# Kernel tuning notes

Hardware: AMD Instinct MI355X
Metric: run time of the kernel (lower is better)

## Reference

```python
import jax, jax.numpy as jnp
import numpy as np

G = 64          # voxel grid side
N_IN = 150000   # input points
N_OUT = 150000  # output points
K = 3           # cubic kernel size
CIN = 32
FOUT = 64


def _make_cloud(rng, n):
    flat = rng.permutation(G ** 3)[:n]
    x = flat % G
    y = (flat // G) % G
    z = flat // (G * G)
    pos = np.stack([x, y, z], axis=-1).astype(np.float32) + 0.5  # voxel centers
    return flat, pos


def setup_inputs() -> dict:
    rng = np.random.default_rng(0)
    flat_in, inp_pos = _make_cloud(rng, N_IN)
    _, out_pos = _make_cloud(np.random.default_rng(1), N_OUT)

    # Fixed-radius (Linf, r = K*voxel*0.51 = 1.53) search on the grid ==
    # 3x3x3 voxel neighborhood lookup. Build dense voxel -> point-index map.
    grid = np.full(G ** 3, -1, dtype=np.int64)
    grid[flat_in] = np.arange(N_IN)
    offs = np.stack(np.meshgrid(*([np.arange(-1, 2)] * 3), indexing='ij'), -1).reshape(-1, 3)  # [27,3]
    out_vox = (out_pos - 0.5).astype(np.int64)              # [M,3]
    nb = out_vox[:, None, :] + offs[None, :, :]             # [M,27,3]
    inb = ((nb >= 0) & (nb < G)).all(-1)                    # [M,27]
    flat = nb[..., 0] + G * nb[..., 1] + G * G * nb[..., 2]
    flat = np.where(inb, flat, 0)
    found = grid[flat]
    mask = inb & (found >= 0)
    nbr_idx = np.where(mask, found, 0).astype(np.int32)

    key = jax.random.key(0)
    k1, k2, k3, k4, k5 = jax.random.split(key, 5)
    return {
        'inp_features': jax.random.normal(k1, (N_IN, CIN), jnp.float32),
        'inp_positions': jnp.asarray(inp_pos),
        'out_positions': jnp.asarray(out_pos),
        'voxel_size': jnp.asarray(1.0, jnp.float32),
        'inp_importance': jax.random.uniform(k2, (N_IN,), jnp.float32),
        'kernel': jax.random.uniform(k3, (K, K, K, CIN, FOUT), jnp.float32, -0.05, 0.05),
        'bias': jnp.zeros((FOUT,), jnp.float32) + 0.01 * jax.random.normal(k4, (FOUT,)),
        'neighbor_index': jnp.asarray(nbr_idx),
        'neighbor_mask': jnp.asarray(mask),
    }


def _sparse_conv(inp_features, inp_positions, out_positions, voxel_size,
                 inp_importance, kernel, bias, neighbor_index, neighbor_mask):
    # offset = 0 (odd kernel). extent = kernel_size * voxel_size.
    extent = K * voxel_size
    nbr_pos = inp_positions[neighbor_index]                  # [M,Kn,3]
    rel = nbr_pos - out_positions[:, None, :]                # [M,Kn,3]
    # identity coordinate mapping: normalize to [-1,1] over the extent
    n = 2.0 * rel / extent
    # align_corners=False mapping to filter coords, + offset (=0)
    fcoord = (n * 0.5 + 0.5) * K - 0.5                        # [M,Kn,3] (x,y,z)
    idx = jnp.clip(jnp.round(fcoord).astype(jnp.int32), 0, K - 1)
    # kernel is indexed [z,y,x,cin,cout]; positions are [x,y,z]
    flat_cell = idx[..., 2] * (K * K) + idx[..., 1] * K + idx[..., 0]   # [M,Kn]
    onehot = jax.nn.one_hot(flat_cell, K ** 3, dtype=inp_features.dtype)  # [M,Kn,27]
    w = (inp_importance[neighbor_index] * neighbor_mask.astype(inp_features.dtype))  # [M,Kn]
    feat = inp_features[neighbor_index] * w[..., None]       # [M,Kn,Cin]
    # accumulate neighbor features into their kernel cell, then contract with kernel
    cellfeat = jnp.einsum('mko,mkc->moc', onehot, feat)      # [M,27,Cin]
    wflat = kernel.reshape(K ** 3, CIN, FOUT)
    out = jnp.einsum('moc,ocf->mf', cellfeat, wflat)         # [M,F]
    return out + bias


def reference(inp_features, inp_positions, out_positions, voxel_size,
              inp_importance, kernel, bias, neighbor_index, neighbor_mask):
    return _sparse_conv(inp_features, inp_positions, out_positions, voxel_size,
                        inp_importance, kernel, bias, neighbor_index, neighbor_mask)
```

## Files before the change

kernel.cpp:

```cpp
#include <hip/hip_runtime.h>
#include <hip/hip_bf16.h>

#define CELLS 27
#define CIN   32
#define FOUT  64
#define M_OUT 150000
#define N_INP 150000
#define GDIM  64
#define NVOX  (GDIM * GDIM * GDIM)

#define GFEAT_SHORTS (NVOX * CIN)
#define GFEAT_BYTES  (GFEAT_SHORTS * 2)
#define OUTMAP_BYTES (NVOX * 4)
#define WT2_SHORTS   (CELLS * 4 * 64 * 8)
#define WT2_BYTES    (WT2_SHORTS * 2)
#define DENSE_WS     ((size_t)GFEAT_BYTES + OUTMAP_BYTES + WT2_BYTES)

#define CHB   16032
#define LDSSZ (4 * CHB)

#define ZROW  N_INP
#define PPG   64
#define GROUPS ((M_OUT + PPG - 1) / PPG)
#define FB_ROWS  (N_INP + 1)
#define FB_BYTES (FB_ROWS * CIN * 2)

typedef __attribute__((ext_vector_type(4))) float f32x4;
typedef __attribute__((ext_vector_type(8))) short bf16x8;

__device__ __forceinline__ short f2bf(float x) {
    union { __hip_bfloat16 h; short s; } u;
    u.h = __float2bfloat16(x);
    return u.s;
}


__global__ __launch_bounds__(256) void build_kernel(const float* __restrict__ feat,
                                                    const float* __restrict__ ipos,
                                                    const float* __restrict__ opos,
                                                    const float* __restrict__ imp,
                                                    const float* __restrict__ W,
                                                    unsigned short* __restrict__ gfeat,
                                                    int* __restrict__ outmap,
                                                    unsigned short* __restrict__ Wt2) {
    int t = blockIdx.x * 256 + threadIdx.x;
    if (t < N_INP * 4) {
        int p = t >> 2, c = t & 3;
        int x = (int)ipos[p * 3 + 0];
        int y = (int)ipos[p * 3 + 1];
        int z = (int)ipos[p * 3 + 2];
        int flat = x + (y << 6) + (z << 12);
        float wv = imp[p];
        const float* fp = feat + (size_t)p * CIN + c * 8;
        f32x4 f0 = *(const f32x4*)fp;
        f32x4 f1 = *(const f32x4*)(fp + 4);
        bf16x8 o;
        o[0] = f2bf(f0.x * wv); o[1] = f2bf(f0.y * wv);
        o[2] = f2bf(f0.z * wv); o[3] = f2bf(f0.w * wv);
        o[4] = f2bf(f1.x * wv); o[5] = f2bf(f1.y * wv);
        o[6] = f2bf(f1.z * wv); o[7] = f2bf(f1.w * wv);
        *(bf16x8*)(gfeat + (size_t)flat * CIN + c * 8) = o;
    } else if (t < N_INP * 4 + M_OUT) {
        int m = t - N_INP * 4;
        int x = (int)opos[m * 3 + 0];
        int y = (int)opos[m * 3 + 1];
        int z = (int)opos[m * 3 + 2];
        outmap[x + (y << 6) + (z << 12)] = m;
    } else {
        int v = t - (N_INP * 4 + M_OUT);
        if (v < CELLS * 4 * 64) {
            int l    = v & 63;
            int ct   = v >> 6;
            int tt   = ct & 3;
            int cell = ct >> 2;
            int fout = tt * 16 + (l & 15);
            int cin0 = (l >> 4) * 8;
            bf16x8 o;
#pragma unroll
            for (int j = 0; j < 8; ++j)
                o[j] = f2bf(W[cell * 2048 + (cin0 + j) * 64 + fout]);
            *(bf16x8*)(Wt2 + (size_t)v * 8) = o;
        }
    }
}

__global__ __launch_bounds__(512, 4) void conv_dense8_kernel(
        const unsigned short* __restrict__ gfeat,
        const int*   __restrict__ outmap,
        const unsigned short* __restrict__ Wt2,
        const float* __restrict__ bias,
        float* __restrict__ out) {
    __shared__ __align__(16) unsigned char sh[LDSSZ];

    const int tid = threadIdx.x;
    const int bid = blockIdx.x;
    const int bx0 = (bid & 7) * 8;
    const int by0 = ((bid >> 3) & 7) * 8;
    const int bz0 = (bid >> 6) * 8;

    bf16x8 hv[8];
#pragma unroll
    for (int it = 0; it < 8; ++it) {
        int c = it * 512 + tid;
        bf16x8 val = {0, 0, 0, 0, 0, 0, 0, 0};
        if (c < 4000) {
            int v = c >> 2, ch = c & 3;
            int q10  = (v * 6554) >> 16;
            int hx   = v - q10 * 10;
            int q100 = (q10 * 6554) >> 16;
            int hy   = q10 - q100 * 10;
            int hz   = q100;
            int gx = bx0 - 1 + hx, gy = by0 - 1 + hy, gz = bz0 - 1 + hz;
            if (((unsigned)gx < 64u) & ((unsigned)gy < 64u) & ((unsigned)gz < 64u)) {
                int flat = gx + (gy << 6) + (gz << 12);
                val = *(const bf16x8*)(gfeat + (size_t)flat * CIN + ch * 8);
            }
        }
        hv[it] = val;
    }
#pragma unroll
    for (int it = 0; it < 8; ++it) {
        int c = it * 512 + tid;
        if (c < 4000) {
            int v = c >> 2, ch = c & 3;
            *(bf16x8*)&sh[ch * CHB + v * 16] = hv[it];
        }
    }
    __syncthreads();

    const int w    = tid >> 6;
    const int lane = tid & 63;
    const int r = lane & 15;
    const int g = lane >> 4;

    const unsigned char* Ab = sh + g * CHB + ((r & 7) + (r >> 3) * 10 + w * 100) * 16;
    const unsigned short* Bp = Wt2 + lane * 8;

    f32x4 acc[4][4];
#pragma unroll
    for (int mt = 0; mt < 4; ++mt)
#pragma unroll
        for (int nt = 0; nt < 4; ++nt) acc[mt][nt] = (f32x4){0.f, 0.f, 0.f, 0.f};

    bf16x8 bb[2][4];
#pragma unroll
    for (int nt = 0; nt < 4; ++nt)
        bb[0][nt] = *(const bf16x8*)(Bp + nt * 512);

#pragma unroll
    for (int cell = 0; cell < CELLS; ++cell) {
        const int cur = cell & 1, nxt = cur ^ 1;
        const int cx = cell % 3, cy = (cell / 3) % 3, cz = cell / 9;
        if (cell + 1 < CELLS) {
#pragma unroll
            for (int nt = 0; nt < 4; ++nt)
                bb[nxt][nt] = *(const bf16x8*)(Bp + (cell + 1) * 2048 + nt * 512);
        }
#pragma unroll
        for (int mt = 0; mt < 4; ++mt) {
            bf16x8 a = *(const bf16x8*)(Ab + (cx + (cy + 2 * mt) * 10 + cz * 100) * 16);
#pragma unroll
            for (int nt = 0; nt < 4; ++nt)
                acc[mt][nt] = __builtin_amdgcn_mfma_f32_16x16x32_bf16(a, bb[cur][nt],
                                                                      acc[mt][nt], 0, 0, 0);
        }
    }

    float bv0 = bias[r], bv1 = bias[16 + r], bv2 = bias[32 + r], bv3 = bias[48 + r];
#pragma unroll
    for (int mt = 0; mt < 4; ++mt) {
#pragma unroll
        for (int j = 0; j < 4; ++j) {
            int p  = mt * 16 + g * 4 + j;
            int px = p & 7, py = p >> 3;
            int om = outmap[(bx0 + px) + ((by0 + py) << 6) + ((bz0 + w) << 12)];
            if (om >= 0) {
                float* op = out + (size_t)om * FOUT + r;
                op[0]  = acc[mt][0][j] + bv0;
                op[16] = acc[mt][1][j] + bv1;
                op[32] = acc[mt][2][j] + bv2;
                op[48] = acc[mt][3][j] + bv3;
            }
        }
    }
}


#define CELL_OF(k) (((k) % 3) * 9 + (((k) / 3) % 3) * 3 + ((k) / 9))

__global__ __launch_bounds__(256) void prep_fb_kernel(const float* __restrict__ W,
                                                      const float* __restrict__ feat,
                                                      const float* __restrict__ imp,
                                                      unsigned short* __restrict__ Wt2,
                                                      unsigned short* __restrict__ fb) {
    int t = blockIdx.x * 256 + threadIdx.x;
    if (t < FB_ROWS * 4) {
        int i = t >> 2, c = t & 3;
        bf16x8 o = {0, 0, 0, 0, 0, 0, 0, 0};
        if (i < N_INP) {
            float w = imp[i];
            const float* fp = feat + (size_t)i * CIN + c * 8;
            f32x4 f0 = *(const f32x4*)fp;
            f32x4 f1 = *(const f32x4*)(fp + 4);
            o[0] = f2bf(f0.x * w); o[1] = f2bf(f0.y * w);
            o[2] = f2bf(f0.z * w); o[3] = f2bf(f0.w * w);
            o[4] = f2bf(f1.x * w); o[5] = f2bf(f1.y * w);
            o[6] = f2bf(f1.z * w); o[7] = f2bf(f1.w * w);
        }
        *(bf16x8*)(fb + (size_t)i * CIN + c * 8) = o;
    } else {
        int v = t - FB_ROWS * 4;
        if (v < CELLS * 4 * 64) {
            int l    = v & 63;
            int ct   = v >> 6;
            int tt   = ct & 3;
            int cell = ct >> 2;
            int fout = tt * 16 + (l & 15);
            int cin0 = (l >> 4) * 8;
            bf16x8 o;
#pragma unroll
            for (int j = 0; j < 8; ++j)
                o[j] = f2bf(W[cell * 2048 + (cin0 + j) * 64 + fout]);
            *(bf16x8*)(Wt2 + (size_t)v * 8) = o;
        }
    }
}

__global__ __launch_bounds__(128, 4) void conv64_kernel(
        const float* __restrict__ opos,
        const float* __restrict__ ipos,
        const int*   __restrict__ nbr,
        const unsigned short* __restrict__ Wt2,
        const unsigned short* __restrict__ fb,
        const float* __restrict__ bias,
        float* __restrict__ out) {
    __shared__ int s_idx[PPG][28];
    __shared__ int s_vox[PPG];
    __shared__ __align__(16) unsigned char s_A[2][4 * 1056];

    const int tid   = threadIdx.x;
    const int lane  = tid & 63;
    const int fhalf = tid >> 6;
    const int m0    = blockIdx.x * PPG;

    const int vx0 = (int)ipos[0];
    const int vy0 = (int)ipos[1];
    const int vz0 = (int)ipos[2];

    if (fhalf == 0) {
        int m = m0 + lane;
        int vp = -1;
        if (m < M_OUT) {
            vp = ((int)opos[m * 3 + 0] + 1) |
                 (((int)opos[m * 3 + 1] + 1) << 8) |
                 (((int)opos[m * 3 + 2] + 1) << 16);
        }
        s_vox[lane] = vp;
    }
    __syncthreads();

#pragma unroll
    for (int it = 0; it < 14; ++it) {
        int e = it * 128 + tid;
        if (e < CELLS * PPG) {
            int p = e / CELLS;
            int k = e - p * CELLS;
            int m = m0 + p;
            int id = (m < M_OUT) ? nbr[m * CELLS + k] : 0;
            int ox = k / 9, oy = (k / 3) % 3, oz = k % 3;
            int tgt = (vx0 - ox + 2) | ((vy0 - oy + 2) << 8) | ((vz0 - oz + 2) << 16);
            bool valid = (id != 0) | (s_vox[p] == tgt);
            s_idx[p][k] = valid ? id : ZROW;
        }
    }
    __syncthreads();

    const int st_c  = lane & 3;
    const int st_r0 = fhalf * 32 + (lane >> 2);
    const int st_r1 = st_r0 + 16;
    const unsigned short* fb_c = fb + st_c * 8;

    const int g = lane >> 4;
    const int r = lane & 15;
    const int wbase = fhalf * 2;

    {
        int i0 = s_idx[st_r0][0];
        int i1 = s_idx[st_r1][0];
        bf16x8 v0 = *(const bf16x8*)(fb_c + (size_t)i0 * CIN);
        bf16x8 v1 = *(const bf16x8*)(fb_c + (size_t)i1 * CIN);
        *(bf16x8*)&s_A[0][st_c * 1056 + st_r0 * 16] = v0;
        *(bf16x8*)&s_A[0][st_c * 1056 + st_r1 * 16] = v1;
    }
    bf16x8 cb0 = *(const bf16x8*)(Wt2 + (CELL_OF(0) * 4 + wbase + 0) * 512 + lane * 8);
    bf16x8 cb1 = *(const bf16x8*)(Wt2 + (CELL_OF(0) * 4 + wbase + 1) * 512 + lane * 8);
    __syncthreads();

    f32x4 acc[8];
#pragma unroll
    for (int i = 0; i < 8; ++i) acc[i] = (f32x4){0.f, 0.f, 0.f, 0.f};

#pragma unroll
    for (int k = 0; k < CELLS; ++k) {
        const int b = k & 1;
        bf16x8 v0, v1, nb0, nb1;
        const bool more = (k + 1 < CELLS);
        if (more) {
            int i0 = s_idx[st_r0][k + 1];
            int i1 = s_idx[st_r1][k + 1];
            v0 = *(const bf16x8*)(fb_c + (size_t)i0 * CIN);
            v1 = *(const bf16x8*)(fb_c + (size_t)i1 * CIN);
            const int c2 = CELL_OF(k + 1);
            nb0 = *(const bf16x8*)(Wt2 + (c2 * 4 + wbase + 0) * 512 + lane * 8);
            nb1 = *(const bf16x8*)(Wt2 + (c2 * 4 + wbase + 1) * 512 + lane * 8);
        }
        const unsigned char* Ab = &s_A[b][0];
        bf16x8 a0 = *(const bf16x8*)(Ab + g * 1056 +   0 + r * 16);
        bf16x8 a1 = *(const bf16x8*)(Ab + g * 1056 + 256 + r * 16);
        bf16x8 a2 = *(const bf16x8*)(Ab + g * 1056 + 512 + r * 16);
        bf16x8 a3 = *(const bf16x8*)(Ab + g * 1056 + 768 + r * 16);
        acc[0] = __builtin_amdgcn_mfma_f32_16x16x32_bf16(a0, cb0, acc[0], 0, 0, 0);
        acc[1] = __builtin_amdgcn_mfma_f32_16x16x32_bf16(a0, cb1, acc[1], 0, 0, 0);
        acc[2] = __builtin_amdgcn_mfma_f32_16x16x32_bf16(a1, cb0, acc[2], 0, 0, 0);
        acc[3] = __builtin_amdgcn_mfma_f32_16x16x32_bf16(a1, cb1, acc[3], 0, 0, 0);
        acc[4] = __builtin_amdgcn_mfma_f32_16x16x32_bf16(a2, cb0, acc[4], 0, 0, 0);
        acc[5] = __builtin_amdgcn_mfma_f32_16x16x32_bf16(a2, cb1, acc[5], 0, 0, 0);
        acc[6] = __builtin_amdgcn_mfma_f32_16x16x32_bf16(a3, cb0, acc[6], 0, 0, 0);
        acc[7] = __builtin_amdgcn_mfma_f32_16x16x32_bf16(a3, cb1, acc[7], 0, 0, 0);
        if (more) {
            *(bf16x8*)&s_A[b ^ 1][st_c * 1056 + st_r0 * 16] = v0;
            *(bf16x8*)&s_A[b ^ 1][st_c * 1056 + st_r1 * 16] = v1;
            cb0 = nb0;
            cb1 = nb1;
        }
        __syncthreads();
    }

    float bb0 = bias[fhalf * 32 + r];
    float bb1 = bias[fhalf * 32 + 16 + r];
#pragma unroll
    for (int h = 0; h < 4; ++h) {
        int base = m0 + h * 16 + 4 * g;
#pragma unroll
        for (int j = 0; j < 4; ++j) {
            int m = base + j;
            if (m < M_OUT) {
                float* op = out + (size_t)m * FOUT + fhalf * 32 + r;
                op[0]  = acc[h * 2 + 0][j] + bb0;
                op[16] = acc[h * 2 + 1][j] + bb1;
            }
        }
    }
}


extern "C" void kernel_launch(void* const* d_in, const int* in_sizes, int n_in,
                              void* d_out, int out_size, void* d_ws, size_t ws_size,
                              hipStream_t stream) {
    const float* feat = (const float*)d_in[0];
    const float* ipos = (const float*)d_in[1];
    const float* opos = (const float*)d_in[2];
    const float* imp  = (const float*)d_in[4];
    const float* W    = (const float*)d_in[5];
    const float* bias = (const float*)d_in[6];
    const int*   nbr  = (const int*)d_in[7];
    float* out = (float*)d_out;

    if (ws_size >= DENSE_WS) {
        unsigned short* gfeat = (unsigned short*)d_ws;
        int* outmap = (int*)((char*)d_ws + GFEAT_BYTES);
        unsigned short* Wt2 = (unsigned short*)((char*)d_ws + GFEAT_BYTES + OUTMAP_BYTES);

        hipMemsetAsync(gfeat, 0x00, GFEAT_BYTES, stream);
        hipMemsetAsync(outmap, 0xFF, OUTMAP_BYTES, stream);
        int build_threads = N_INP * 4 + M_OUT + CELLS * 4 * 64;
        hipLaunchKernelGGL(build_kernel, dim3((build_threads + 255) / 256), dim3(256),
                           0, stream, feat, ipos, opos, imp, W, gfeat, outmap, Wt2);
        hipLaunchKernelGGL(conv_dense8_kernel, dim3(512), dim3(512), 0, stream,
                           gfeat, outmap, Wt2, bias, out);
    } else {
        unsigned short* Wt2 = (unsigned short*)d_ws;
        unsigned short* fb  = (unsigned short*)((char*)d_ws + WT2_BYTES);
        int prep_threads = FB_ROWS * 4 + CELLS * 4 * 64;
        hipLaunchKernelGGL(prep_fb_kernel, dim3((prep_threads + 255) / 256), dim3(256),
                           0, stream, W, feat, imp, Wt2, fb);
        hipLaunchKernelGGL(conv64_kernel, dim3(GROUPS), dim3(128), 0, stream,
                           opos, ipos, nbr, Wt2, fb, bias, out);
    }
}
```

Before: 156.9 us.

## Stage per-cell weight tiles through double-buffered LDS instead of per-wave global loads

```diff
diff --git a/kernel.cpp b/kernel.cpp
--- a/kernel.cpp
+++ b/kernel.cpp
@@ -16,8 +16,10 @@
 #define WT2_BYTES    (WT2_SHORTS * 2)
 #define DENSE_WS     ((size_t)GFEAT_BYTES + OUTMAP_BYTES + WT2_BYTES)
 
-#define CHB   16032
-#define LDSSZ (4 * CHB)
+#define CHB      16032
+#define BBUF0    (4 * CHB)
+#define BBUFSZ   4128
+#define LDSSZ    (BBUF0 + 2 * BBUFSZ)
 
 #define ZROW  N_INP
 #define PPG   64
@@ -100,32 +102,38 @@
 
     bf16x8 hv[8];
 #pragma unroll
-    for (int it = 0; it < 8; ++it) {
-        int c = it * 512 + tid;
-        bf16x8 val = {0, 0, 0, 0, 0, 0, 0, 0};
-        if (c < 4000) {
-            int v = c >> 2, ch = c & 3;
-            int q10  = (v * 6554) >> 16;
-            int hx   = v - q10 * 10;
-            int q100 = (q10 * 6554) >> 16;
-            int hy   = q10 - q100 * 10;
-            int hz   = q100;
-            int gx = bx0 - 1 + hx, gy = by0 - 1 + hy, gz = bz0 - 1 + hz;
-            if (((unsigned)gx < 64u) & ((unsigned)gy < 64u) & ((unsigned)gz < 64u)) {
-                int flat = gx + (gy << 6) + (gz << 12);
-                val = *(const bf16x8*)(gfeat + (size_t)flat * CIN + ch * 8);
+    for (int ch = 0; ch < 4; ++ch) {
+#pragma unroll
+        for (int h = 0; h < 2; ++h) {
+            int v = h * 512 + tid;
+            bf16x8 val = {0, 0, 0, 0, 0, 0, 0, 0};
+            if (v < 1000) {
+                int q10  = (v * 6554) >> 16;
+                int hx   = v - q10 * 10;
+                int q100 = (q10 * 6554) >> 16;
+                int hy   = q10 - q100 * 10;
+                int hz   = q100;
+                int gx = bx0 - 1 + hx, gy = by0 - 1 + hy, gz = bz0 - 1 + hz;
+                if (((unsigned)gx < 64u) & ((unsigned)gy < 64u) & ((unsigned)gz < 64u)) {
+                    int flat = gx + (gy << 6) + (gz << 12);
+                    val = *(const bf16x8*)(gfeat + (size_t)flat * CIN + ch * 8);
+                }
             }
-        }
-        hv[it] = val;
-    }
-#pragma unroll
-    for (int it = 0; it < 8; ++it) {
-        int c = it * 512 + tid;
-        if (c < 4000) {
-            int v = c >> 2, ch = c & 3;
-            *(bf16x8*)&sh[ch * CHB + v * 16] = hv[it];
-        }
-    }
+            hv[ch * 2 + h] = val;
+        }
+    }
+    bf16x8 b0stage;
+    if (tid < 256) b0stage = *(const bf16x8*)(Wt2 + tid * 8);
+#pragma unroll
+    for (int ch = 0; ch < 4; ++ch) {
+#pragma unroll
+        for (int h = 0; h < 2; ++h) {
+            int v = h * 512 + tid;
+            if (v < 1000)
+                *(bf16x8*)&sh[ch * CHB + v * 16] = hv[ch * 2 + h];
+        }
+    }
+    if (tid < 256) *(bf16x8*)&sh[BBUF0 + tid * 16] = b0stage;
     __syncthreads();
 
     const int w    = tid >> 6;
@@ -134,36 +142,45 @@
     const int g = lane >> 4;
 
     const unsigned char* Ab = sh + g * CHB + ((r & 7) + (r >> 3) * 10 + w * 100) * 16;
-    const unsigned short* Bp = Wt2 + lane * 8;
+    const unsigned char* Bb = sh + BBUF0 + lane * 16;
 
     f32x4 acc[4][4];
 #pragma unroll
     for (int mt = 0; mt < 4; ++mt)
 #pragma unroll
         for (int nt = 0; nt < 4; ++nt) acc[mt][nt] = (f32x4){0.f, 0.f, 0.f, 0.f};
-
-    bf16x8 bb[2][4];
-#pragma unroll
-    for (int nt = 0; nt < 4; ++nt)
-        bb[0][nt] = *(const bf16x8*)(Bp + nt * 512);
 
 #pragma unroll
     for (int cell = 0; cell < CELLS; ++cell) {
         const int cur = cell & 1, nxt = cur ^ 1;
         const int cx = cell % 3, cy = (cell / 3) % 3, cz = cell / 9;
-        if (cell + 1 < CELLS) {
+        const bool more = (cell + 1 < CELLS);
+
+        bf16x8 stg;
+        if (more && tid < 256)
+            stg = *(const bf16x8*)(Wt2 + (cell + 1) * 2048 + tid * 8);
+
+        bf16x8 b[4];
+#pragma unroll
+        for (int nt = 0; nt < 4; ++nt)
+            b[nt] = *(const bf16x8*)(Bb + cur * BBUFSZ + nt * 1024);
+
+        bf16x8 a0 = *(const bf16x8*)(Ab + (cx + (cy + 0) * 10 + cz * 100) * 16);
+#pragma unroll
+        for (int mt = 0; mt < 4; ++mt) {
+            bf16x8 a1;
+            if (mt < 3)
+                a1 = *(const bf16x8*)(Ab + (cx + (cy + 2 * (mt + 1)) * 10 + cz * 100) * 16);
 #pragma unroll
             for (int nt = 0; nt < 4; ++nt)
-                bb[nxt][nt] = *(const bf16x8*)(Bp + (cell + 1) * 2048 + nt * 512);
-        }
-#pragma unroll
-        for (int mt = 0; mt < 4; ++mt) {
-            bf16x8 a = *(const bf16x8*)(Ab + (cx + (cy + 2 * mt) * 10 + cz * 100) * 16);
-#pragma unroll
-            for (int nt = 0; nt < 4; ++nt)
-                acc[mt][nt] = __builtin_amdgcn_mfma_f32_16x16x32_bf16(a, bb[cur][nt],
+                acc[mt][nt] = __builtin_amdgcn_mfma_f32_16x16x32_bf16(a0, b[nt],
                                                                       acc[mt][nt], 0, 0, 0);
-        }
+            a0 = a1;
+        }
+
+        if (more && tid < 256)
+            *(bf16x8*)&sh[BBUF0 + nxt * BBUFSZ + tid * 16] = stg;
+        if (more) __syncthreads();
     }
 
     float bv0 = bias[r], bv1 = bias[16 + r], bv2 = bias[32 + r], bv3 = bias[48 + r];
```

Measured after the change: 158.3 us. Within noise of the previous version (+0.9%).
